# Performance work log

Measured on AMD Instinct MI355X. Metric: run time of the kernel, lower is better.

Reference implementation:

```python
import jax, jax.numpy as jnp
import numpy as np

B, N, D = 16, 4096, 64
LB_TH = 0.01
L2_LAMDA = 0.001
RECONS_LAMDA = 0.2


def _xavier(key, shape):
    fan_in, fan_out = shape[0], shape[1]
    a = float(np.sqrt(6.0 / (fan_in + fan_out)))
    return jax.random.uniform(key, shape, jnp.float32, -a, a)


def setup_inputs() -> dict:
    key = jax.random.key(0)
    k1, k2, k3 = jax.random.split(key, 3)
    X = jax.random.normal(k1, (B, N, D), jnp.float32)
    r_proj = _xavier(k2, (D, D))
    incidence_m = _xavier(k3, (N, N - 1))
    return {"X": X, "r_proj": r_proj, "incidence_m": incidence_m}


def reference(X, r_proj, incidence_m):
    n = incidence_m.shape[0]
    # clamp(min=lb_th) followed by masked_fill(~(v > lb_th), 0) == keep only orig > lb_th
    w = jnp.where(incidence_m > LB_TH, incidence_m, jnp.zeros((), X.dtype))  # [N, N-1]
    # scatter each row's N-1 weights into an NxN matrix, skipping the diagonal
    rows = jnp.arange(n)[:, None]                      # [N,1]
    cols = jnp.arange(n - 1)[None, :]                  # [1,N-1]
    full_cols = cols + (cols >= rows).astype(cols.dtype)  # [N,N-1]
    W = jnp.zeros((n, n), X.dtype).at[rows, full_cols].set(w)
    # per-node projection of master node features: X @ r_proj
    X_proj = jnp.einsum('bnd,de->bne', X, r_proj)      # [B,N,D]
    # neighbor reconstruction for every node at once
    recon = jnp.einsum('ij,bjd->bid', W, X)            # [B,N,D]
    recon_err = jnp.sqrt(jnp.sum((X_proj - recon) ** 2, axis=-1))  # [B,N]
    l1 = jnp.max(jnp.abs(w), axis=1)                   # [N] (max over single-row sum == max abs)
    l2 = jnp.sqrt(jnp.sum(w ** 2, axis=1))             # [N]
    recon_loss = recon_err * RECONS_LAMDA + l1[None, :] + L2_LAMDA * l2[None, :]
    incidence_all = W + jnp.eye(n, dtype=X.dtype)
    return recon_loss, incidence_all
```

## Files before the change

### kernel.cpp

```cpp
#include <hip/hip_runtime.h>
#include <hip/hip_bf16.h>

#define BB 16
#define NN 4096
#define DD 64
#define NM1 4095

typedef __bf16 bf16x8 __attribute__((ext_vector_type(8)));
typedef float f32x4 __attribute__((ext_vector_type(4)));

typedef __attribute__((address_space(1))) const void gas_void;
typedef __attribute__((address_space(3))) void las_void;


__global__ __launch_bounds__(256) void build_kernel(
    const float* __restrict__ inc, float* __restrict__ out_inc,
    __bf16* __restrict__ A16, float* __restrict__ mxa, float* __restrict__ ssa)
{
    int t = threadIdx.x;
    int base = blockIdx.x << 12;
    int rA = (int)((unsigned)base / NM1);
    float pm0 = 0.f, ps0 = 0.f, pm1 = 0.f, ps1 = 0.f;
    #pragma unroll
    for (int j = 0; j < 16; ++j) {
        int f = base + j * 256 + t;
        int i = (int)((unsigned)f / NM1);
        int c = f - i * NM1;
        float x = inc[f];
        float w = x > 0.01f ? x : 0.f;
        int dst = f + i + (c >= i);
        out_inc[dst] = w;
        A16[dst] = (__bf16)w;
        if (i == rA) { pm0 = fmaxf(pm0, w); ps0 += w * w; }
        else         { pm1 = fmaxf(pm1, w); ps1 += w * w; }
    }
    #pragma unroll
    for (int off = 32; off; off >>= 1) {
        pm0 = fmaxf(pm0, __shfl_down(pm0, off));
        ps0 += __shfl_down(ps0, off);
        pm1 = fmaxf(pm1, __shfl_down(pm1, off));
        ps1 += __shfl_down(ps1, off);
    }
    __shared__ float sm0[4], sq0[4], sm1[4], sq1[4];
    int wid = t >> 6;
    if ((t & 63) == 0) { sm0[wid] = pm0; sq0[wid] = ps0; sm1[wid] = pm1; sq1[wid] = ps1; }
    __syncthreads();
    if (t == 0) {
        float m0v = fmaxf(fmaxf(sm0[0], sm0[1]), fmaxf(sm0[2], sm0[3]));
        float s0v = sq0[0] + sq0[1] + sq0[2] + sq0[3];
        float m1v = fmaxf(fmaxf(sm1[0], sm1[1]), fmaxf(sm1[2], sm1[3]));
        float s1v = sq1[0] + sq1[1] + sq1[2] + sq1[3];
        atomicMax((unsigned*)(mxa + rA), __float_as_uint(m0v));
        atomicAdd(ssa + rA, s0v);
        int rB = rA + 1;
        if (rB < NN) {
            atomicMax((unsigned*)(mxa + rB), __float_as_uint(m1v));
            atomicAdd(ssa + rB, s1v);
        }
    }
}

__global__ __launch_bounds__(256) void xt_kernel(
    const float* __restrict__ X, __bf16* __restrict__ XT,
    float* __restrict__ out_inc, __bf16* __restrict__ A16)
{
    __shared__ __bf16 tile[64 * 72];
    int t = threadIdx.x;
    int ntile = blockIdx.x, b = blockIdx.y;
    int n = t >> 2, q = t & 3;
    const float* src = X + ((size_t)b * NN + ntile * 64 + n) * DD + q * 16;
    #pragma unroll
    for (int v = 0; v < 4; ++v) {
        f32x4 u = *(const f32x4*)(src + v * 4);
        #pragma unroll
        for (int j = 0; j < 4; ++j) {
            int d = q * 16 + v * 4 + j;
            tile[d * 72 + n] = (__bf16)u[j];
        }
    }
    __syncthreads();
    int d = t >> 2;
    __bf16* dst = XT + ((size_t)b * DD + d) * NN + ntile * 64 + q * 16;
    *(bf16x8*)dst       = *(bf16x8*)&tile[d * 72 + q * 16];
    *(bf16x8*)(dst + 8) = *(bf16x8*)&tile[d * 72 + q * 16 + 8];
    if (b == 0 && t < 64) {
        int r = ntile * 64 + t;
        out_inc[(size_t)r * NN + r] = 1.0f;
        A16[(size_t)r * NN + r] = (__bf16)1.0f;
    }
}

__global__ __launch_bounds__(256, 1) void gemm_loss_kernel(
    const __bf16* __restrict__ A16, const __bf16* __restrict__ XT,
    const float* __restrict__ X, const float* __restrict__ rproj,
    const float* __restrict__ mxa, const float* __restrict__ ssa,
    float* __restrict__ loss)
{
    __shared__ __bf16 smem[4 * 16384];

    const int t = threadIdx.x;
    const int wave = t >> 6, lane = t & 63;
    const int quad = lane >> 4, ln = lane & 15;
    const int sr = lane >> 3, so = lane & 7;
    const int bq = wave >> 1;
    const int wr = (wave & 1) << 6;
    const int m0 = blockIdx.x * 128;
    const int b0 = blockIdx.y * 2;

    const __bf16* Abase = A16 + (size_t)m0 * NN;
    const __bf16* XTb   = XT + (size_t)b0 * DD * NN;

    f32x4 acc[4][4];
    f32x4 zero = {0.f, 0.f, 0.f, 0.f};
    #pragma unroll
    for (int mt = 0; mt < 4; ++mt)
        #pragma unroll
        for (int ct = 0; ct < 4; ++ct) acc[mt][ct] = zero;

    auto stage = [&](int buf, int kt) {
        __bf16* bA = smem + buf * 16384;
        __bf16* bX = bA + 8192;
        const int k0 = kt << 6;
        #pragma unroll
        for (int p = 0; p < 4; ++p) {
            const int r0 = (p << 5) + (wave << 3);
            const int r  = r0 + sr;
            const int og = so ^ (r & 7);
            __builtin_amdgcn_global_load_lds(
                (gas_void*)(Abase + (size_t)r * NN + k0 + (og << 3)),
                (las_void*)(bA + r0 * 64), 16, 0, 0);
            __builtin_amdgcn_global_load_lds(
                (gas_void*)(XTb + (size_t)r * NN + k0 + (og << 3)),
                (las_void*)(bX + r0 * 64), 16, 0, 0);
        }
    };

    auto compute = [&](int buf) {
        const __bf16* bA = smem + buf * 16384;
        const __bf16* bX = bA + 8192 + (bq << 12);
        #pragma unroll
        for (int kk = 0; kk < 64; kk += 32) {
            const int oc = (kk >> 3) + quad;
            bf16x8 af[4], bfr[4];
            #pragma unroll
            for (int mt = 0; mt < 4; ++mt) {
                const int r = wr + mt * 16 + ln;
                af[mt] = *(const bf16x8*)&bA[r * 64 + ((oc ^ (r & 7)) << 3)];
            }
            #pragma unroll
            for (int ct = 0; ct < 4; ++ct) {
                const int n = ct * 16 + ln;
                bfr[ct] = *(const bf16x8*)&bX[n * 64 + ((oc ^ (n & 7)) << 3)];
            }
            #pragma unroll
            for (int mt = 0; mt < 4; ++mt)
                #pragma unroll
                for (int ct = 0; ct < 4; ++ct)
                    acc[mt][ct] = __builtin_amdgcn_mfma_f32_16x16x32_bf16(
                        af[mt], bfr[ct], acc[mt][ct], 0, 0, 0);
        }
    };

    const int NT = NN / 64;
    stage(0, 0);
    stage(1, 1);
    stage(2, 2);
    for (int kt = 0; kt < NT; ++kt) {
        const int nx = kt + 3;
        if (nx < NT) {
            stage(nx & 3, nx);
            asm volatile("s_waitcnt vmcnt(24)" ::: "memory");
        } else if (kt == NT - 3) {
            asm volatile("s_waitcnt vmcnt(16)" ::: "memory");
        } else if (kt == NT - 2) {
            asm volatile("s_waitcnt vmcnt(8)" ::: "memory");
        } else {
            asm volatile("s_waitcnt vmcnt(0)" ::: "memory");
        }
        __builtin_amdgcn_s_barrier();
        compute(kt & 3);
        asm volatile("" ::: "memory");
        __builtin_amdgcn_s_barrier();
    }

    {
        const int rr = t >> 1, q = t & 1;
        #pragma unroll
        for (int bb = 0; bb < 2; ++bb) {
            const float* xs = X + ((size_t)(b0 + bb) * NN + m0 + rr) * DD + q * 32;
            __bf16* XA = smem + bb * 8192;
            #pragma unroll
            for (int v = 0; v < 4; ++v) {
                f32x4 u0 = *(const f32x4*)(xs + v * 8);
                f32x4 u1 = *(const f32x4*)(xs + v * 8 + 4);
                bf16x8 w;
                #pragma unroll
                for (int j = 0; j < 4; ++j) { w[j] = (__bf16)u0[j]; w[j + 4] = (__bf16)u1[j]; }
                const int o = (q * 4 + v) ^ (rr & 7);
                *(bf16x8*)&XA[rr * 64 + o * 8] = w;
            }
        }
        {
            const int rr2 = t >> 2, q2 = t & 3;
            const float* rs = rproj + (size_t)rr2 * DD + q2 * 16;
            __bf16* R = smem + 16384;
            #pragma unroll
            for (int v = 0; v < 4; ++v) {
                f32x4 u = *(const f32x4*)(rs + v * 4);
                #pragma unroll
                for (int j = 0; j < 4; ++j) {
                    const int d = q2 * 16 + v * 4 + j;
                    float val = u[j] + (d == rr2 ? 1.0f : 0.0f);
                    R[d * 64 + (((rr2 >> 3) ^ (d & 7)) << 3) + (rr2 & 7)] = (__bf16)val;
                }
            }
        }
    }
    __syncthreads();

    #pragma unroll
    for (int mt = 0; mt < 4; ++mt)
        #pragma unroll
        for (int ct = 0; ct < 4; ++ct) acc[mt][ct] = -acc[mt][ct];

    {
        const __bf16* XA = smem + bq * 8192;
        const __bf16* R  = smem + 16384;
        #pragma unroll
        for (int kk = 0; kk < DD; kk += 32) {
            const int oc = (kk >> 3) + quad;
            bf16x8 af[4], bfr[4];
            #pragma unroll
            for (int mt = 0; mt < 4; ++mt) {
                const int r = wr + mt * 16 + ln;
                af[mt] = *(const bf16x8*)&XA[r * 64 + ((oc ^ (r & 7)) << 3)];
            }
            #pragma unroll
            for (int ct = 0; ct < 4; ++ct) {
                const int n = ct * 16 + ln;
                bfr[ct] = *(const bf16x8*)&R[n * 64 + ((oc ^ (n & 7)) << 3)];
            }
            #pragma unroll
            for (int mt = 0; mt < 4; ++mt)
                #pragma unroll
                for (int ct = 0; ct < 4; ++ct)
                    acc[mt][ct] = __builtin_amdgcn_mfma_f32_16x16x32_bf16(
                        af[mt], bfr[ct], acc[mt][ct], 0, 0, 0);
        }
    }

    #pragma unroll
    for (int mt = 0; mt < 4; ++mt) {
        #pragma unroll
        for (int rg = 0; rg < 4; ++rg) {
            float s = 0.f;
            #pragma unroll
            for (int ct = 0; ct < 4; ++ct) {
                float d = acc[mt][ct][rg];
                s += d * d;
            }
            s += __shfl_xor(s, 1);
            s += __shfl_xor(s, 2);
            s += __shfl_xor(s, 4);
            s += __shfl_xor(s, 8);
            if (ln == 0) {
                int row = m0 + wr + mt * 16 + quad * 4 + rg;
                loss[(size_t)(b0 + bq) * NN + row] =
                    0.2f * sqrtf(s) + mxa[row] + 0.001f * sqrtf(ssa[row]);
            }
        }
    }
}

extern "C" void kernel_launch(void* const* d_in, const int* in_sizes, int n_in,
                              void* d_out, int out_size, void* d_ws, size_t ws_size,
                              hipStream_t stream) {
    const float* X   = (const float*)d_in[0];
    const float* r   = (const float*)d_in[1];
    const float* inc = (const float*)d_in[2];
    float* out      = (float*)d_out;
    float* out_loss = out;
    float* out_inc  = out + (size_t)BB * NN;

    char* ws = (char*)d_ws;
    float*  mxa = (float*)ws;
    float*  ssa = (float*)(ws + 16384);
    __bf16* XT  = (__bf16*)(ws + 32768);
    __bf16* A16 = (__bf16*)(ws + 32768 + (size_t)8 * 1024 * 1024);

    hipMemsetAsync(mxa, 0, 32768, stream);

    hipLaunchKernelGGL(build_kernel, dim3(NM1), dim3(256), 0, stream,
                       inc, out_inc, A16, mxa, ssa);
    hipLaunchKernelGGL(xt_kernel, dim3(NN / 64, BB), dim3(256), 0, stream,
                       X, XT, out_inc, A16);
    hipLaunchKernelGGL(gemm_loss_kernel, dim3(NN / 128, BB / 2), dim3(256), 0, stream,
                       A16, XT, X, r, mxa, ssa, out_loss);
}
```

Before: 195.7 us.

## Split GEMM K-tile across two wave groups with 512 threads and LDS reduction

The GEMM+loss kernel now runs 8 waves per block instead of 4. Each half of the waves handles one 32-wide half of every 64-wide K tile, and the partial accumulators are summed through LDS before the epilogue. The pipeline drops the trailing barrier per iteration, issues the next stage after compute, and raises wave priority around the MFMA block. This adds latency hiding and MFMA issue parallelism per CU, at the cost of an LDS reduction step and higher register pressure under the 512-thread launch bound.

```diff
diff --git a/kernel.cpp b/kernel.cpp
--- a/kernel.cpp
+++ b/kernel.cpp
@@ -90,7 +90,7 @@
     }
 }
 
-__global__ __launch_bounds__(256, 1) void gemm_loss_kernel(
+__global__ __launch_bounds__(512, 1) void gemm_loss_kernel(
     const __bf16* __restrict__ A16, const __bf16* __restrict__ XT,
     const float* __restrict__ X, const float* __restrict__ rproj,
     const float* __restrict__ mxa, const float* __restrict__ ssa,
@@ -102,8 +102,9 @@
     const int wave = t >> 6, lane = t & 63;
     const int quad = lane >> 4, ln = lane & 15;
     const int sr = lane >> 3, so = lane & 7;
-    const int bq = wave >> 1;
-    const int wr = (wave & 1) << 6;
+    const int kh  = wave >> 2;
+    const int bq  = (wave >> 1) & 1;
+    const int wrh = (wave & 1) << 6;
     const int m0 = blockIdx.x * 128;
     const int b0 = blockIdx.y * 2;
 
@@ -122,8 +123,8 @@
         __bf16* bX = bA + 8192;
         const int k0 = kt << 6;
         #pragma unroll
-        for (int p = 0; p < 4; ++p) {
-            const int r0 = (p << 5) + (wave << 3);
+        for (int p = 0; p < 2; ++p) {
+            const int r0 = (p << 6) + (wave << 3);
             const int r  = r0 + sr;
             const int og = so ^ (r & 7);
             __builtin_amdgcn_global_load_lds(
@@ -138,69 +139,92 @@
     auto compute = [&](int buf) {
         const __bf16* bA = smem + buf * 16384;
         const __bf16* bX = bA + 8192 + (bq << 12);
-        #pragma unroll
-        for (int kk = 0; kk < 64; kk += 32) {
-            const int oc = (kk >> 3) + quad;
-            bf16x8 af[4], bfr[4];
-            #pragma unroll
-            for (int mt = 0; mt < 4; ++mt) {
-                const int r = wr + mt * 16 + ln;
-                af[mt] = *(const bf16x8*)&bA[r * 64 + ((oc ^ (r & 7)) << 3)];
-            }
-            #pragma unroll
-            for (int ct = 0; ct < 4; ++ct) {
-                const int n = ct * 16 + ln;
-                bfr[ct] = *(const bf16x8*)&bX[n * 64 + ((oc ^ (n & 7)) << 3)];
-            }
+        const int oc = (kh << 2) + quad;
+        bf16x8 af[4], bfr[4];
+        #pragma unroll
+        for (int mt = 0; mt < 4; ++mt) {
+            const int r = wrh + mt * 16 + ln;
+            af[mt] = *(const bf16x8*)&bA[r * 64 + ((oc ^ (r & 7)) << 3)];
+        }
+        #pragma unroll
+        for (int ct = 0; ct < 4; ++ct) {
+            const int n = ct * 16 + ln;
+            bfr[ct] = *(const bf16x8*)&bX[n * 64 + ((oc ^ (n & 7)) << 3)];
+        }
+        __builtin_amdgcn_s_setprio(1);
+        #pragma unroll
+        for (int mt = 0; mt < 4; ++mt)
+            #pragma unroll
+            for (int ct = 0; ct < 4; ++ct)
+                acc[mt][ct] = __builtin_amdgcn_mfma_f32_16x16x32_bf16(
+                    af[mt], bfr[ct], acc[mt][ct], 0, 0, 0);
+        __builtin_amdgcn_s_setprio(0);
+    };
+
+#define FENCE() asm volatile("" ::: "memory")
+#define VMCNT(N) asm volatile("s_waitcnt vmcnt(" #N ")" ::: "memory")
+#define BAR() do { __builtin_amdgcn_s_barrier(); \
+                   __builtin_amdgcn_sched_barrier(0); } while (0)
+
+    const int NT = NN / 64;
+    stage(0, 0); FENCE();
+    stage(1, 1); FENCE();
+    stage(2, 2); FENCE();
+    for (int kt = 0; kt < NT - 3; ++kt) {
+        VMCNT(8);
+        BAR();
+        compute(kt & 3);
+        stage((kt + 3) & 3, kt + 3);
+    }
+    VMCNT(8);  BAR(); compute(1);
+    VMCNT(4);  BAR(); compute(2);
+    VMCNT(0);  BAR(); compute(3);
+
+#undef BAR
+#undef VMCNT
+#undef FENCE
+
+    __syncthreads();
+    {
+        float* red = (float*)smem;
+        if (kh == 1) {
+            float* dst = red + (wave & 3) * 4096;
             #pragma unroll
             for (int mt = 0; mt < 4; ++mt)
                 #pragma unroll
                 for (int ct = 0; ct < 4; ++ct)
-                    acc[mt][ct] = __builtin_amdgcn_mfma_f32_16x16x32_bf16(
-                        af[mt], bfr[ct], acc[mt][ct], 0, 0, 0);
-        }
-    };
-
-    const int NT = NN / 64;
-    stage(0, 0);
-    stage(1, 1);
-    stage(2, 2);
-    for (int kt = 0; kt < NT; ++kt) {
-        const int nx = kt + 3;
-        if (nx < NT) {
-            stage(nx & 3, nx);
-            asm volatile("s_waitcnt vmcnt(24)" ::: "memory");
-        } else if (kt == NT - 3) {
-            asm volatile("s_waitcnt vmcnt(16)" ::: "memory");
-        } else if (kt == NT - 2) {
-            asm volatile("s_waitcnt vmcnt(8)" ::: "memory");
-        } else {
-            asm volatile("s_waitcnt vmcnt(0)" ::: "memory");
-        }
-        __builtin_amdgcn_s_barrier();
-        compute(kt & 3);
-        asm volatile("" ::: "memory");
-        __builtin_amdgcn_s_barrier();
+                    *(f32x4*)&dst[(mt * 4 + ct) * 256 + lane * 4] = acc[mt][ct];
+        }
+        __syncthreads();
+        if (kh == 0) {
+            const float* src = red + (wave & 3) * 4096;
+            #pragma unroll
+            for (int mt = 0; mt < 4; ++mt)
+                #pragma unroll
+                for (int ct = 0; ct < 4; ++ct)
+                    acc[mt][ct] += *(const f32x4*)&src[(mt * 4 + ct) * 256 + lane * 4];
+        }
+        __syncthreads();
     }
 
     {
-        const int rr = t >> 1, q = t & 1;
+        const int rr = t >> 2, q = t & 3;
         #pragma unroll
         for (int bb = 0; bb < 2; ++bb) {
-            const float* xs = X + ((size_t)(b0 + bb) * NN + m0 + rr) * DD + q * 32;
+            const float* xs = X + ((size_t)(b0 + bb) * NN + m0 + rr) * DD + q * 16;
             __bf16* XA = smem + bb * 8192;
             #pragma unroll
-            for (int v = 0; v < 4; ++v) {
+            for (int v = 0; v < 2; ++v) {
                 f32x4 u0 = *(const f32x4*)(xs + v * 8);
                 f32x4 u1 = *(const f32x4*)(xs + v * 8 + 4);
                 bf16x8 w;
                 #pragma unroll
                 for (int j = 0; j < 4; ++j) { w[j] = (__bf16)u0[j]; w[j + 4] = (__bf16)u1[j]; }
-                const int o = (q * 4 + v) ^ (rr & 7);
+                const int o = (q * 2 + v) ^ (rr & 7);
                 *(bf16x8*)&XA[rr * 64 + o * 8] = w;
             }
         }
-        {
+        if (t < 256) {
             const int rr2 = t >> 2, q2 = t & 3;
             const float* rs = rproj + (size_t)rr2 * DD + q2 * 16;
             __bf16* R = smem + 16384;
@@ -218,21 +242,21 @@
     }
     __syncthreads();
 
-    #pragma unroll
-    for (int mt = 0; mt < 4; ++mt)
-        #pragma unroll
-        for (int ct = 0; ct < 4; ++ct) acc[mt][ct] = -acc[mt][ct];
-
-    {
+    if (kh == 0) {
+        #pragma unroll
+        for (int mt = 0; mt < 4; ++mt)
+            #pragma unroll
+            for (int ct = 0; ct < 4; ++ct) acc[mt][ct] = -acc[mt][ct];
+
         const __bf16* XA = smem + bq * 8192;
         const __bf16* R  = smem + 16384;
         #pragma unroll
-        for (int kk = 0; kk < DD; kk += 32) {
-            const int oc = (kk >> 3) + quad;
+        for (int h = 0; h < 2; ++h) {
+            const int oc = (h << 2) + quad;
             bf16x8 af[4], bfr[4];
             #pragma unroll
             for (int mt = 0; mt < 4; ++mt) {
-                const int r = wr + mt * 16 + ln;
+                const int r = wrh + mt * 16 + ln;
                 af[mt] = *(const bf16x8*)&XA[r * 64 + ((oc ^ (r & 7)) << 3)];
             }
             #pragma unroll
@@ -247,26 +271,26 @@
                     acc[mt][ct] = __builtin_amdgcn_mfma_f32_16x16x32_bf16(
                         af[mt], bfr[ct], acc[mt][ct], 0, 0, 0);
         }
-    }
-
-    #pragma unroll
-    for (int mt = 0; mt < 4; ++mt) {
-        #pragma unroll
-        for (int rg = 0; rg < 4; ++rg) {
-            float s = 0.f;
-            #pragma unroll
-            for (int ct = 0; ct < 4; ++ct) {
-                float d = acc[mt][ct][rg];
-                s += d * d;
-            }
-            s += __shfl_xor(s, 1);
-            s += __shfl_xor(s, 2);
-            s += __shfl_xor(s, 4);
-            s += __shfl_xor(s, 8);
-            if (ln == 0) {
-                int row = m0 + wr + mt * 16 + quad * 4 + rg;
-                loss[(size_t)(b0 + bq) * NN + row] =
-                    0.2f * sqrtf(s) + mxa[row] + 0.001f * sqrtf(ssa[row]);
+
+        #pragma unroll
+        for (int mt = 0; mt < 4; ++mt) {
+            #pragma unroll
+            for (int rg = 0; rg < 4; ++rg) {
+                float s = 0.f;
+                #pragma unroll
+                for (int ct = 0; ct < 4; ++ct) {
+                    float d = acc[mt][ct][rg];
+                    s += d * d;
+                }
+                s += __shfl_xor(s, 1);
+                s += __shfl_xor(s, 2);
+                s += __shfl_xor(s, 4);
+                s += __shfl_xor(s, 8);
+                if (ln == 0) {
+                    int row = m0 + wrh + mt * 16 + quad * 4 + rg;
+                    loss[(size_t)(b0 + bq) * NN + row] =
+                        0.2f * sqrtf(s) + mxa[row] + 0.001f * sqrtf(ssa[row]);
+                }
             }
         }
     }
@@ -294,6 +318,6 @@
                        inc, out_inc, A16, mxa, ssa);
     hipLaunchKernelGGL(xt_kernel, dim3(NN / 64, BB), dim3(256), 0, stream,
                        X, XT, out_inc, A16);
-    hipLaunchKernelGGL(gemm_loss_kernel, dim3(NN / 128, BB / 2), dim3(256), 0, stream,
+    hipLaunchKernelGGL(gemm_loss_kernel, dim3(NN / 128, BB / 2), dim3(512), 0, stream,
                        A16, XT, X, r, mxa, ssa, out_loss);
 }
```

Result: faster. 186.1 us (-4.9%).
